# Kernel optimization log

Hardware: AMD Instinct MI355X
Metric: run time of the kernel (lower is better)

The kernel has to match this reference:

```python
import jax, jax.numpy as jnp
import numpy as np

DEPTH = 6
B, D, E, H = 8192, 256, 256, 50
N_INNER = (1 << (DEPTH - 1)) - 1   # 31
N_LEAF = 1 << (DEPTH - 1)          # 32


def setup_inputs() -> dict:
    key = jax.random.key(0)
    ks = jax.random.split(key, 16)
    g = lambda k, shape, fan: (jax.random.normal(k, shape, dtype=jnp.float32)
                               / jnp.sqrt(jnp.float32(fan)))
    return {
        "x": jax.random.normal(ks[0], (B, D), dtype=jnp.float32),
        "enc_W": g(ks[1], (4, E, E), E),
        "enc_b": jnp.zeros((4, E), jnp.float32),
        # inner nodes, stacked over N_INNER
        "in_W1": g(ks[2], (N_INNER, E, H), E),
        "in_b1": jnp.zeros((N_INNER, H), jnp.float32),
        "in_Ww": g(ks[3], (N_INNER, H, D), H),
        "in_bw": jnp.zeros((N_INNER, D), jnp.float32),
        "in_Wb": g(ks[4], (N_INNER, H), H),
        "in_bb": jnp.zeros((N_INNER,), jnp.float32),
        "in_Wbeta": g(ks[5], (N_INNER, H), H),
        "in_bbeta": jnp.zeros((N_INNER,), jnp.float32),
        # leaf models, stacked over N_LEAF
        "lf_W1": g(ks[6], (N_LEAF, E, E), E),
        "lf_b1": jnp.zeros((N_LEAF, E), jnp.float32),
        "lf_W2": g(ks[7], (N_LEAF, E), E),
        "lf_b2": jnp.zeros((N_LEAF,), jnp.float32),
    }


def reference(x, enc_W, enc_b, in_W1, in_b1, in_Ww, in_bw, in_Wb, in_bb,
              in_Wbeta, in_bbeta, lf_W1, lf_b1, lf_W2, lf_b2):
    batch = x.shape[0]
    # encoder: 4 relu Dense layers
    emb = x
    for i in range(4):
        emb = jax.nn.relu(emb @ enc_W[i] + enc_b[i])

    # all inner-node gates in one batched pass  -> pR: [N_INNER, B]
    h = jax.nn.relu(jnp.einsum('be,neh->nbh', emb, in_W1) + in_b1[:, None, :])
    w = jax.nn.softmax(jnp.einsum('nbh,nhd->nbd', h, in_Ww) + in_bw[:, None, :], axis=-1)
    b = jnp.einsum('nbh,nh->nb', h, in_Wb) + in_bb[:, None]
    beta = jnp.einsum('nbh,nh->nb', h, in_Wbeta) + in_bbeta[:, None]
    pR = jax.nn.sigmoid(beta * (jnp.einsum('nbd,bd->nb', w, x) + b))

    # all leaf MLPs in one batched pass  -> y_leaf: [N_LEAF, B]
    hl = jax.nn.relu(jnp.einsum('be,leh->lbh', emb, lf_W1) + lf_b1[:, None, :])
    y_leaf = jnp.einsum('lbh,lh->lb', hl, lf_W2) + lf_b2[:, None]

    # path probabilities (heap ordering; right child weighted by pR)
    prob = jnp.ones((batch, 1), dtype=x.dtype)
    idx = 0
    for level in range(DEPTH - 1):
        cnt = 1 << level
        p = pR[idx:idx + cnt].T                       # [B, cnt]
        prob = jnp.stack([prob * (1.0 - p), prob * p], axis=-1).reshape(batch, 2 * cnt)
        idx += cnt

    return jnp.sum(prob * y_leaf.T, axis=1, keepdims=True)  # [B, 1]
```

## Files before the change

kernel.cpp:

```cpp
#include <hip/hip_runtime.h>


#define B_ROWS 8192
#define HDIM 50
#define HPAD 64

typedef _Float16 f16;
typedef _Float16 f16x8 __attribute__((ext_vector_type(8)));
typedef _Float16 f16x4 __attribute__((ext_vector_type(4)));
typedef float f32x4 __attribute__((ext_vector_type(4)));

static __device__ __forceinline__ f32x4 mfma16(f16x8 a, f16x8 b, f32x4 c) {
  return __builtin_amdgcn_mfma_f32_16x16x32_f16(a, b, c, 0, 0, 0);
}

static __device__ __forceinline__ void gload16(const void* g, void* l) {
  __builtin_amdgcn_global_load_lds(
      (const __attribute__((address_space(1))) unsigned int*)g,
      (__attribute__((address_space(3))) unsigned int*)l, 16, 0, 0);
}

__global__ void k_cast_f16(const float* __restrict__ in, f16* __restrict__ out, int n4) {
  int i = blockIdx.x * blockDim.x + threadIdx.x;
  if (i < n4) {
    float4 v = reinterpret_cast<const float4*>(in)[i];
    f16x4 o = { (f16)v.x, (f16)v.y, (f16)v.z, (f16)v.w };
    reinterpret_cast<f16x4*>(out)[i] = o;
  }
}

__global__ void k_tcast(const float* __restrict__ in, f16* __restrict__ out,
                        int R, int C, int Rp, int Cp) {
  __shared__ float t[32][33];
  const int s = blockIdx.z;
  const int r0 = blockIdx.x * 32, c0 = blockIdx.y * 32;
  const int tx = threadIdx.x, ty = threadIdx.y;
  const float* ip = in + (size_t)s * R * C;
  f16* op = out + (size_t)s * Cp * Rp;
#pragma unroll
  for (int i = 0; i < 4; ++i) {
    int r = r0 + ty + 8 * i, c = c0 + tx;
    t[ty + 8 * i][tx] = (r < R && c < C) ? ip[(size_t)r * C + c] : 0.f;
  }
  __syncthreads();
#pragma unroll
  for (int i = 0; i < 4; ++i) {
    int c = c0 + ty + 8 * i, r = r0 + tx;
    if (c < Cp && r < Rp) op[(size_t)c * Rp + r] = (f16)t[tx][ty + 8 * i];
  }
}

__global__ __launch_bounds__(256) void k_enc4(const float* __restrict__ x,
    const f16* __restrict__ encWT, const float* __restrict__ enc_b,
    f16* __restrict__ emb) {
  __shared__ f16 act[2][32][264];
  __shared__ f16 Bt[256][72];
  const int tid = threadIdx.x;
  const int wave = tid >> 6, lane = tid & 63;
  const int grp = lane >> 4, lid = lane & 15;
  const int row0 = blockIdx.x * 32;
  const int sr = tid >> 3, sc = (tid & 7) * 8;

  {
    const int xr = tid >> 3, xc = (tid & 7) * 32;
    const float* src = x + (size_t)(row0 + xr) * 256 + xc;
#pragma unroll
    for (int j = 0; j < 4; ++j) {
      float4 a = ((const float4*)src)[2 * j];
      float4 b = ((const float4*)src)[2 * j + 1];
      f16x8 o = { (f16)a.x, (f16)a.y, (f16)a.z, (f16)a.w,
                  (f16)b.x, (f16)b.y, (f16)b.z, (f16)b.w };
      *(f16x8*)&act[0][xr][xc + 8 * j] = o;
    }
  }
  __syncthreads();

  for (int l = 0; l < 4; ++l) {
    const int cur = l & 1, nxt = cur ^ 1;
    f32x4 acc[2][4] = {};
    for (int kt = 0; kt < 4; ++kt) {
#pragma unroll
      for (int p = 0; p < 8; ++p)
        *(f16x8*)&Bt[p * 32 + sr][sc] =
            *(const f16x8*)&encWT[(size_t)l * 65536 + (size_t)(p * 32 + sr) * 256 + kt * 64 + sc];
      __syncthreads();
#pragma unroll
      for (int kk = 0; kk < 2; ++kk) {
        f16x8 af[2], bf[4];
#pragma unroll
        for (int m = 0; m < 2; ++m)
          af[m] = *(const f16x8*)&act[cur][m * 16 + lid][kt * 64 + kk * 32 + grp * 8];
#pragma unroll
        for (int n = 0; n < 4; ++n)
          bf[n] = *(const f16x8*)&Bt[wave * 64 + n * 16 + lid][kk * 32 + grp * 8];
#pragma unroll
        for (int m = 0; m < 2; ++m)
#pragma unroll
          for (int n = 0; n < 4; ++n) acc[m][n] = mfma16(af[m], bf[n], acc[m][n]);
      }
      __syncthreads();
    }
#pragma unroll
    for (int n = 0; n < 4; ++n) {
      const int col = wave * 64 + n * 16 + lid;
      const float bv = enc_b[l * 256 + col];
#pragma unroll
      for (int m = 0; m < 2; ++m)
#pragma unroll
        for (int r = 0; r < 4; ++r) {
          float v = acc[m][n][r] + bv;
          act[nxt][m * 16 + grp * 4 + r][col] = (f16)(v > 0.f ? v : 0.f);
        }
    }
    __syncthreads();
  }
  {
    const int xr = tid >> 3, xc = (tid & 7) * 32;
#pragma unroll
    for (int j = 0; j < 4; ++j)
      *(f16x8*)&emb[(size_t)(row0 + xr) * 256 + xc + 8 * j] =
          *(const f16x8*)&act[0][xr][xc + 8 * j];
  }
}

__global__ __launch_bounds__(256, 2) void k_inner(const f16* __restrict__ emb,
    const f16* __restrict__ W1T_all, const float* __restrict__ b1_all,
    const f16* __restrict__ WwT_all, const f16* __restrict__ x_h,
    const float* __restrict__ bw_all, const float* __restrict__ Wb_all,
    const float* __restrict__ bb_all, const float* __restrict__ Wbeta_all,
    const float* __restrict__ bbeta_all, float* __restrict__ pR) {
  __shared__ f16 et[64][264];
  __shared__ f16 hbuf[4][64][72];
  __shared__ float bbuf[4][64], betabuf[4][64];

  const int tid = threadIdx.x;
  const int wave = tid >> 6, lane = tid & 63;
  const int grp = lane >> 4, lid = lane & 15;
  const int row0 = blockIdx.x * 64;
  const int node = blockIdx.y * 4 + wave;

  {
    const int r = tid >> 2, cb = (tid & 3) * 64;
#pragma unroll
    for (int j = 0; j < 8; ++j)
      *(f16x8*)&et[r][cb + 8 * j] =
          *(const f16x8*)&emb[(size_t)(row0 + r) * 256 + cb + 8 * j];
  }
  __syncthreads();
  if (node >= 31) return;

  const f16* W1T = W1T_all + (size_t)node * HPAD * 256;
  const f16* WwT = WwT_all + (size_t)node * 256 * HPAD;

  f32x4 acc1[4][4] = {};
  f16x8 wf[2][4];
#pragma unroll
  for (int h4 = 0; h4 < 4; ++h4)
    wf[0][h4] = *(const f16x8*)&W1T[(size_t)(h4 * 16 + lid) * 256 + grp * 8];
  for (int kt = 0; kt < 8; ++kt) {
    const int cur = kt & 1, nxt = cur ^ 1;
    if (kt < 7) {
#pragma unroll
      for (int h4 = 0; h4 < 4; ++h4)
        wf[nxt][h4] = *(const f16x8*)&W1T[(size_t)(h4 * 16 + lid) * 256 +
                                          (kt + 1) * 32 + grp * 8];
    }
    f16x8 af[4];
#pragma unroll
    for (int m = 0; m < 4; ++m)
      af[m] = *(const f16x8*)&et[m * 16 + lid][kt * 32 + grp * 8];
#pragma unroll
    for (int h4 = 0; h4 < 4; ++h4)
#pragma unroll
      for (int m = 0; m < 4; ++m)
        acc1[h4][m] = mfma16(wf[cur][h4], af[m], acc1[h4][m]);
  }
#pragma unroll
  for (int h4 = 0; h4 < 4; ++h4) {
    const int hc = h4 * 16 + grp * 4;
    float bva[4];
#pragma unroll
    for (int r = 0; r < 4; ++r)
      bva[r] = (hc + r < HDIM) ? b1_all[node * HDIM + hc + r] : 0.f;
#pragma unroll
    for (int m = 0; m < 4; ++m) {
      f16x4 hv;
#pragma unroll
      for (int r = 0; r < 4; ++r) {
        float v = acc1[h4][m][r] + bva[r];
        hv[r] = (f16)(v > 0.f ? v : 0.f);
      }
      *(f16x4*)&hbuf[wave][m * 16 + lid][hc] = hv;
    }
  }

  {
    float sb = 0.f, sbt = 0.f;
#pragma unroll
    for (int v8 = 0; v8 < 7; ++v8) {
      f16x8 hv = *(const f16x8*)&hbuf[wave][lane][v8 * 8];
#pragma unroll
      for (int j = 0; j < 8; ++j) {
        const int c = v8 * 8 + j;
        if (c < HDIM) {
          float hvf = (float)hv[j];
          sb  += hvf * Wb_all[node * HDIM + c];
          sbt += hvf * Wbeta_all[node * HDIM + c];
        }
      }
    }
    bbuf[wave][lane] = sb + bb_all[node];
    betabuf[wave][lane] = sbt + bbeta_all[node];
  }

  float s[4] = {0.f, 0.f, 0.f, 0.f}, dt[4] = {0.f, 0.f, 0.f, 0.f};
  for (int c = 0; c < 4; ++c) {
    f16x8 awf[2][4];
#pragma unroll
    for (int kk = 0; kk < 2; ++kk)
#pragma unroll
      for (int n4 = 0; n4 < 4; ++n4)
        awf[kk][n4] = *(const f16x8*)&WwT[(size_t)(c * 64 + n4 * 16 + lid) * HPAD +
                                          kk * 32 + grp * 8];
    f32x4 acc2[4][4] = {};
#pragma unroll
    for (int kk = 0; kk < 2; ++kk) {
      f16x8 hf[4];
#pragma unroll
      for (int m = 0; m < 4; ++m)
        hf[m] = *(const f16x8*)&hbuf[wave][m * 16 + lid][kk * 32 + grp * 8];
#pragma unroll
      for (int n4 = 0; n4 < 4; ++n4)
#pragma unroll
        for (int m = 0; m < 4; ++m)
          acc2[n4][m] = mfma16(awf[kk][n4], hf[m], acc2[n4][m]);
    }
#pragma unroll
    for (int n4 = 0; n4 < 4; ++n4) {
      float4 bwv = *(const float4*)&bw_all[node * 256 + c * 64 + n4 * 16 + grp * 4];
      float bwa[4] = {bwv.x, bwv.y, bwv.z, bwv.w};
#pragma unroll
      for (int m = 0; m < 4; ++m) {
        f16x4 xv = *(const f16x4*)&x_h[(size_t)(row0 + m * 16 + lid) * 256 +
                                       c * 64 + n4 * 16 + grp * 4];
#pragma unroll
        for (int r = 0; r < 4; ++r) {
          float e = __expf(acc2[n4][m][r] + bwa[r]);
          s[m] += e;
          dt[m] += e * (float)xv[r];
        }
      }
    }
  }
#pragma unroll
  for (int m = 0; m < 4; ++m) {
    s[m]  += __shfl_xor(s[m], 16, 64);  s[m]  += __shfl_xor(s[m], 32, 64);
    dt[m] += __shfl_xor(dt[m], 16, 64); dt[m] += __shfl_xor(dt[m], 32, 64);
  }
  if (grp == 0) {
#pragma unroll
    for (int m = 0; m < 4; ++m) {
      const int row = m * 16 + lid;
      float z = betabuf[wave][row] * (dt[m] / s[m] + bbuf[wave][row]);
      pR[(size_t)(row0 + row) * 32 + node] = 1.f / (1.f + __expf(-z));
    }
  }
}

__global__ __launch_bounds__(512) void k_leaf(const f16* __restrict__ emb,
    const f16* __restrict__ W1T_all, const float* __restrict__ b1_all,
    const float* __restrict__ W2_all, const float* __restrict__ b2_all,
    float* __restrict__ y_leaf) {
  __shared__ f16 Alds[128 * 64];
  __shared__ f16 Blds[256 * 64];
  __shared__ float red[4][128];
  const int tid = threadIdx.x;
  const int wave = tid >> 6, lane = tid & 63;
  const int wm = wave >> 2, wn = wave & 3;
  const int grp = lane >> 4, lid = lane & 15;
  const int row0 = blockIdx.x * 128;
  const int leaf = blockIdx.y;
  const f16* WT = W1T_all + (size_t)leaf * 65536;
  const float* b1 = b1_all + leaf * 256;
  const float* W2 = W2_all + leaf * 256;

  const int lrow = lane >> 3;
  const int sslot = (lane & 7) ^ lrow;

  f32x4 acc[4][4] = {};
  const int swzA = (lid & 7);
  for (int kt = 0; kt < 4; ++kt) {
#pragma unroll
    for (int r2 = 0; r2 < 2; ++r2) {
      const int arow = r2 * 64 + wave * 8 + lrow;
      gload16(emb + (size_t)(row0 + arow) * 256 + kt * 64 + sslot * 8,
              (char*)Alds + r2 * 8192 + wave * 1024);
    }
#pragma unroll
    for (int r4 = 0; r4 < 4; ++r4) {
      const int brow = r4 * 64 + wave * 8 + lrow;
      gload16(WT + (size_t)brow * 256 + kt * 64 + sslot * 8,
              (char*)Blds + r4 * 8192 + wave * 1024);
    }
    __syncthreads();
#pragma unroll
    for (int kk = 0; kk < 2; ++kk) {
      f16x8 af[4], bf[4];
#pragma unroll
      for (int rb = 0; rb < 4; ++rb) {
        const int row = wm * 64 + rb * 16 + lid;
        af[rb] = *(const f16x8*)((const char*)Alds + row * 128 +
                                 (((kk * 4 + grp) ^ swzA) << 4));
      }
#pragma unroll
      for (int cb = 0; cb < 4; ++cb) {
        const int row = wn * 64 + cb * 16 + lid;
        bf[cb] = *(const f16x8*)((const char*)Blds + row * 128 +
                                 (((kk * 4 + grp) ^ swzA) << 4));
      }
#pragma unroll
      for (int cb = 0; cb < 4; ++cb)
#pragma unroll
        for (int rb = 0; rb < 4; ++rb)
          acc[cb][rb] = mfma16(bf[cb], af[rb], acc[cb][rb]);
    }
    __syncthreads();
  }
  float b1a[4][4], w2a[4][4];
#pragma unroll
  for (int cb = 0; cb < 4; ++cb) {
    float4 t1 = *(const float4*)&b1[wn * 64 + cb * 16 + grp * 4];
    float4 t2 = *(const float4*)&W2[wn * 64 + cb * 16 + grp * 4];
    b1a[cb][0] = t1.x; b1a[cb][1] = t1.y; b1a[cb][2] = t1.z; b1a[cb][3] = t1.w;
    w2a[cb][0] = t2.x; w2a[cb][1] = t2.y; w2a[cb][2] = t2.z; w2a[cb][3] = t2.w;
  }
  float rs[4] = {0.f, 0.f, 0.f, 0.f};
#pragma unroll
  for (int cb = 0; cb < 4; ++cb)
#pragma unroll
    for (int rb = 0; rb < 4; ++rb)
#pragma unroll
      for (int r = 0; r < 4; ++r) {
        float v = acc[cb][rb][r] + b1a[cb][r];
        v = v > 0.f ? v : 0.f;
        rs[rb] += v * w2a[cb][r];
      }
#pragma unroll
  for (int rb = 0; rb < 4; ++rb) {
    rs[rb] += __shfl_xor(rs[rb], 16, 64);
    rs[rb] += __shfl_xor(rs[rb], 32, 64);
  }
  if (lane < 16)
#pragma unroll
    for (int rb = 0; rb < 4; ++rb)
      red[wn][wm * 64 + rb * 16 + lane] = rs[rb];
  __syncthreads();
  if (tid < 128) {
    float y = red[0][tid] + red[1][tid] + red[2][tid] + red[3][tid] + b2_all[leaf];
    y_leaf[(size_t)(row0 + tid) * 32 + leaf] = y;
  }
}

__global__ void k_combine(const float* __restrict__ pR, const float* __restrict__ y_leaf,
                          float* __restrict__ out) {
  const int b = blockIdx.x * 256 + threadIdx.x;
  float p[32], y[32];
  const float4* pp = (const float4*)(pR + (size_t)b * 32);
  const float4* yp = (const float4*)(y_leaf + (size_t)b * 32);
#pragma unroll
  for (int i = 0; i < 8; ++i) {
    float4 v = pp[i]; p[i*4] = v.x; p[i*4+1] = v.y; p[i*4+2] = v.z; p[i*4+3] = v.w;
    float4 w = yp[i]; y[i*4] = w.x; y[i*4+1] = w.y; y[i*4+2] = w.z; y[i*4+3] = w.w;
  }
  float o = 0.f;
#pragma unroll
  for (int l = 0; l < 32; ++l) {
    float pr = 1.f;
    int node = 0;
#pragma unroll
    for (int k = 0; k < 5; ++k) {
      const int bit = (l >> (4 - k)) & 1;
      const float pv = p[node];
      pr *= bit ? pv : (1.f - pv);
      node = 2 * node + 1 + bit;
    }
    o += pr * y[l];
  }
  out[b] = o;
}

extern "C" void kernel_launch(void* const* d_in, const int* in_sizes, int n_in,
                              void* d_out, int out_size, void* d_ws, size_t ws_size,
                              hipStream_t stream) {
  (void)in_sizes; (void)n_in; (void)out_size; (void)ws_size;
  const float* x        = (const float*)d_in[0];
  const float* enc_W    = (const float*)d_in[1];
  const float* enc_b    = (const float*)d_in[2];
  const float* in_W1    = (const float*)d_in[3];
  const float* in_b1    = (const float*)d_in[4];
  const float* in_Ww    = (const float*)d_in[5];
  const float* in_bw    = (const float*)d_in[6];
  const float* in_Wb    = (const float*)d_in[7];
  const float* in_bb    = (const float*)d_in[8];
  const float* in_Wbeta = (const float*)d_in[9];
  const float* in_bbeta = (const float*)d_in[10];
  const float* lf_W1    = (const float*)d_in[11];
  const float* lf_b1    = (const float*)d_in[12];
  const float* lf_W2    = (const float*)d_in[13];
  const float* lf_b2    = (const float*)d_in[14];
  float* out = (float*)d_out;

  char* ws = (char*)d_ws;
  f16* x_h     = (f16*)(ws);
  f16* emb     = (f16*)(ws + 4194304);
  f16* encWT   = (f16*)(ws + 8388608);
  f16* lfW1T   = (f16*)(ws + 8912896);
  f16* inW1T   = (f16*)(ws + 13107200);
  f16* inWwT   = (f16*)(ws + 14123008);
  float* pR    = (float*)(ws + 15138816);
  float* y_leaf= (float*)(ws + 16187392);

  dim3 tb(32, 8);
  hipLaunchKernelGGL(k_cast_f16, dim3(2048), dim3(256), 0, stream, x, x_h, B_ROWS * 256 / 4);
  hipLaunchKernelGGL(k_tcast, dim3(8, 8, 4),  tb, 0, stream, enc_W, encWT, 256, 256, 256, 256);
  hipLaunchKernelGGL(k_tcast, dim3(8, 8, 32), tb, 0, stream, lf_W1, lfW1T, 256, 256, 256, 256);
  hipLaunchKernelGGL(k_tcast, dim3(8, 2, 31), tb, 0, stream, in_W1, inW1T, 256, 50, 256, 64);
  hipLaunchKernelGGL(k_tcast, dim3(2, 8, 31), tb, 0, stream, in_Ww, inWwT, 50, 256, 64, 256);

  hipLaunchKernelGGL(k_enc4, dim3(256), dim3(256), 0, stream, x, encWT, enc_b, emb);
  hipLaunchKernelGGL(k_inner, dim3(128, 8), dim3(256), 0, stream, emb, inW1T, in_b1,
                     inWwT, x_h, in_bw, in_Wb, in_bb, in_Wbeta, in_bbeta, pR);
  hipLaunchKernelGGL(k_leaf, dim3(64, 32), dim3(512), 0, stream, emb, lfW1T, lf_b1, lf_W2, lf_b2, y_leaf);
  hipLaunchKernelGGL(k_combine, dim3(32), dim3(256), 0, stream, pR, y_leaf, out);
}
```

Baseline: 232.3 us.

## Fold gate heads into MFMA, stage x in LDS, double-buffer larger leaf tiles

The inner-node kernel now computes the b and beta heads as an extra MFMA tile, using a prepacked weight block that appends the Wb and Wbeta rows to the transposed Ww. This replaces the scalar per-lane dot product. It also stages the x tile into the emb LDS buffer so the softmax dot product reads LDS instead of global memory, and keeps the padded waves alive until the final barrier. The leaf kernel doubles its row tile to 256 and double-buffers the async global-to-LDS loads so the next k-slice loads while the current one computes. The cost is more LDS use (about 130KB in the leaf kernel) and more accumulator registers, which may lower occupancy.

```diff
diff --git a/kernel.cpp b/kernel.cpp
--- a/kernel.cpp
+++ b/kernel.cpp
@@ -47,6 +47,32 @@
   for (int i = 0; i < 4; ++i) {
     int c = c0 + ty + 8 * i, r = r0 + tx;
     if (c < Cp && r < Rp) op[(size_t)c * Rp + r] = (f16)t[tx][ty + 8 * i];
+  }
+}
+
+__global__ void k_prep_ww(const float* __restrict__ Ww, const float* __restrict__ Wb,
+                          const float* __restrict__ Wbeta, f16* __restrict__ WwE) {
+  const int node = blockIdx.x;
+  const int d = threadIdx.x;
+  f16 row[64];
+#pragma unroll
+  for (int h = 0; h < 64; ++h)
+    row[h] = (h < HDIM) ? (f16)Ww[((size_t)node * HDIM + h) * 256 + d] : (f16)0.f;
+  f16* dst = WwE + (size_t)node * 272 * 64 + (size_t)d * 64;
+#pragma unroll
+  for (int j = 0; j < 8; ++j) *(f16x8*)&dst[j * 8] = *(const f16x8*)&row[j * 8];
+  if (d < 16) {
+    f16 er[64];
+#pragma unroll
+    for (int h = 0; h < 64; ++h) {
+      float v = 0.f;
+      if (d == 0 && h < HDIM) v = Wb[node * HDIM + h];
+      if (d == 1 && h < HDIM) v = Wbeta[node * HDIM + h];
+      er[h] = (f16)v;
+    }
+    f16* dst2 = WwE + (size_t)node * 272 * 64 + (size_t)(256 + d) * 64;
+#pragma unroll
+    for (int j = 0; j < 8; ++j) *(f16x8*)&dst2[j * 8] = *(const f16x8*)&er[j * 8];
   }
 }
 
@@ -125,19 +151,18 @@
 
 __global__ __launch_bounds__(256, 2) void k_inner(const f16* __restrict__ emb,
     const f16* __restrict__ W1T_all, const float* __restrict__ b1_all,
-    const f16* __restrict__ WwT_all, const f16* __restrict__ x_h,
-    const float* __restrict__ bw_all, const float* __restrict__ Wb_all,
-    const float* __restrict__ bb_all, const float* __restrict__ Wbeta_all,
+    const f16* __restrict__ WwE_all, const f16* __restrict__ x_h,
+    const float* __restrict__ bw_all, const float* __restrict__ bb_all,
     const float* __restrict__ bbeta_all, float* __restrict__ pR) {
   __shared__ f16 et[64][264];
   __shared__ f16 hbuf[4][64][72];
-  __shared__ float bbuf[4][64], betabuf[4][64];
 
   const int tid = threadIdx.x;
   const int wave = tid >> 6, lane = tid & 63;
   const int grp = lane >> 4, lid = lane & 15;
   const int row0 = blockIdx.x * 64;
-  const int node = blockIdx.y * 4 + wave;
+  const int node_raw = blockIdx.y * 4 + wave;
+  const int node = node_raw < 31 ? node_raw : 30;
 
   {
     const int r = tid >> 2, cb = (tid & 3) * 64;
@@ -147,10 +172,9 @@
           *(const f16x8*)&emb[(size_t)(row0 + r) * 256 + cb + 8 * j];
   }
   __syncthreads();
-  if (node >= 31) return;
 
   const f16* W1T = W1T_all + (size_t)node * HPAD * 256;
-  const f16* WwT = WwT_all + (size_t)node * 256 * HPAD;
+  const f16* WwE = WwE_all + (size_t)node * 272 * 64;
 
   f32x4 acc1[4][4] = {};
   f16x8 wf[2][4];
@@ -193,24 +217,25 @@
       *(f16x4*)&hbuf[wave][m * 16 + lid][hc] = hv;
     }
   }
-
+  __syncthreads();
   {
-    float sb = 0.f, sbt = 0.f;
-#pragma unroll
-    for (int v8 = 0; v8 < 7; ++v8) {
-      f16x8 hv = *(const f16x8*)&hbuf[wave][lane][v8 * 8];
-#pragma unroll
-      for (int j = 0; j < 8; ++j) {
-        const int c = v8 * 8 + j;
-        if (c < HDIM) {
-          float hvf = (float)hv[j];
-          sb  += hvf * Wb_all[node * HDIM + c];
-          sbt += hvf * Wbeta_all[node * HDIM + c];
-        }
-      }
-    }
-    bbuf[wave][lane] = sb + bb_all[node];
-    betabuf[wave][lane] = sbt + bbeta_all[node];
+    const int r = tid >> 2, cb = (tid & 3) * 64;
+#pragma unroll
+    for (int j = 0; j < 8; ++j)
+      *(f16x8*)&et[r][cb + 8 * j] =
+          *(const f16x8*)&x_h[(size_t)(row0 + r) * 256 + cb + 8 * j];
+  }
+  __syncthreads();
+
+  f32x4 accm[4] = {};
+#pragma unroll
+  for (int kk = 0; kk < 2; ++kk) {
+    f16x8 wmini = *(const f16x8*)&WwE[(size_t)(256 + lid) * 64 + kk * 32 + grp * 8];
+#pragma unroll
+    for (int m = 0; m < 4; ++m) {
+      f16x8 hf = *(const f16x8*)&hbuf[wave][m * 16 + lid][kk * 32 + grp * 8];
+      accm[m] = mfma16(wmini, hf, accm[m]);
+    }
   }
 
   float s[4] = {0.f, 0.f, 0.f, 0.f}, dt[4] = {0.f, 0.f, 0.f, 0.f};
@@ -220,7 +245,7 @@
     for (int kk = 0; kk < 2; ++kk)
 #pragma unroll
       for (int n4 = 0; n4 < 4; ++n4)
-        awf[kk][n4] = *(const f16x8*)&WwT[(size_t)(c * 64 + n4 * 16 + lid) * HPAD +
+        awf[kk][n4] = *(const f16x8*)&WwE[(size_t)(c * 64 + n4 * 16 + lid) * 64 +
                                           kk * 32 + grp * 8];
     f32x4 acc2[4][4] = {};
 #pragma unroll
@@ -241,8 +266,7 @@
       float bwa[4] = {bwv.x, bwv.y, bwv.z, bwv.w};
 #pragma unroll
       for (int m = 0; m < 4; ++m) {
-        f16x4 xv = *(const f16x4*)&x_h[(size_t)(row0 + m * 16 + lid) * 256 +
-                                       c * 64 + n4 * 16 + grp * 4];
+        f16x4 xv = *(const f16x4*)&et[m * 16 + lid][c * 64 + n4 * 16 + grp * 4];
 #pragma unroll
         for (int r = 0; r < 4; ++r) {
           float e = __expf(acc2[n4][m][r] + bwa[r]);
@@ -257,11 +281,14 @@
     s[m]  += __shfl_xor(s[m], 16, 64);  s[m]  += __shfl_xor(s[m], 32, 64);
     dt[m] += __shfl_xor(dt[m], 16, 64); dt[m] += __shfl_xor(dt[m], 32, 64);
   }
-  if (grp == 0) {
+  if (grp == 0 && node_raw < 31) {
+    const float bbv = bb_all[node], bbetav = bbeta_all[node];
 #pragma unroll
     for (int m = 0; m < 4; ++m) {
       const int row = m * 16 + lid;
-      float z = betabuf[wave][row] * (dt[m] / s[m] + bbuf[wave][row]);
+      float b = accm[m][0] + bbv;
+      float beta = accm[m][1] + bbetav;
+      float z = beta * (dt[m] / s[m] + b);
       pR[(size_t)(row0 + row) * 32 + node] = 1.f / (1.f + __expf(-z));
     }
   }
@@ -271,14 +298,14 @@
     const f16* __restrict__ W1T_all, const float* __restrict__ b1_all,
     const float* __restrict__ W2_all, const float* __restrict__ b2_all,
     float* __restrict__ y_leaf) {
-  __shared__ f16 Alds[128 * 64];
-  __shared__ f16 Blds[256 * 64];
-  __shared__ float red[4][128];
+  __shared__ f16 Albuf[2][256 * 64];
+  __shared__ f16 Blbuf[2][256 * 64];
+  __shared__ float red[4][256];
   const int tid = threadIdx.x;
   const int wave = tid >> 6, lane = tid & 63;
   const int wm = wave >> 2, wn = wave & 3;
   const int grp = lane >> 4, lid = lane & 15;
-  const int row0 = blockIdx.x * 128;
+  const int row0 = blockIdx.x * 256;
   const int leaf = blockIdx.y;
   const f16* WT = W1T_all + (size_t)leaf * 65536;
   const float* b1 = b1_all + leaf * 256;
@@ -286,45 +313,48 @@
 
   const int lrow = lane >> 3;
   const int sslot = (lane & 7) ^ lrow;
-
-  f32x4 acc[4][4] = {};
   const int swzA = (lid & 7);
+
+#define LEAF_STAGE(buf, kt)                                                    \
+  {                                                                            \
+    _Pragma("unroll")                                                          \
+    for (int r4 = 0; r4 < 4; ++r4) {                                           \
+      const int rr = r4 * 64 + wave * 8 + lrow;                                \
+      gload16(emb + (size_t)(row0 + rr) * 256 + (kt) * 64 + sslot * 8,         \
+              (char*)&Albuf[buf][0] + r4 * 8192 + wave * 1024);                \
+      gload16(WT + (size_t)rr * 256 + (kt) * 64 + sslot * 8,                   \
+              (char*)&Blbuf[buf][0] + r4 * 8192 + wave * 1024);                \
+    }                                                                          \
+  }
+
+  f32x4 acc[4][8] = {};
+  LEAF_STAGE(0, 0);
+  __syncthreads();
   for (int kt = 0; kt < 4; ++kt) {
-#pragma unroll
-    for (int r2 = 0; r2 < 2; ++r2) {
-      const int arow = r2 * 64 + wave * 8 + lrow;
-      gload16(emb + (size_t)(row0 + arow) * 256 + kt * 64 + sslot * 8,
-              (char*)Alds + r2 * 8192 + wave * 1024);
-    }
-#pragma unroll
-    for (int r4 = 0; r4 < 4; ++r4) {
-      const int brow = r4 * 64 + wave * 8 + lrow;
-      gload16(WT + (size_t)brow * 256 + kt * 64 + sslot * 8,
-              (char*)Blds + r4 * 8192 + wave * 1024);
-    }
-    __syncthreads();
+    const int b = kt & 1;
+    if (kt < 3) LEAF_STAGE(b ^ 1, kt + 1);
 #pragma unroll
     for (int kk = 0; kk < 2; ++kk) {
-      f16x8 af[4], bf[4];
-#pragma unroll
-      for (int rb = 0; rb < 4; ++rb) {
-        const int row = wm * 64 + rb * 16 + lid;
-        af[rb] = *(const f16x8*)((const char*)Alds + row * 128 +
+      f16x8 af[8], bf[4];
+#pragma unroll
+      for (int rb = 0; rb < 8; ++rb) {
+        const int row = wm * 128 + rb * 16 + lid;
+        af[rb] = *(const f16x8*)((const char*)&Albuf[b][0] + row * 128 +
                                  (((kk * 4 + grp) ^ swzA) << 4));
       }
 #pragma unroll
       for (int cb = 0; cb < 4; ++cb) {
-        const int row = wn * 64 + cb * 16 + lid;
-        bf[cb] = *(const f16x8*)((const char*)Blds + row * 128 +
+        const int col = wn * 64 + cb * 16 + lid;
+        bf[cb] = *(const f16x8*)((const char*)&Blbuf[b][0] + col * 128 +
                                  (((kk * 4 + grp) ^ swzA) << 4));
       }
 #pragma unroll
       for (int cb = 0; cb < 4; ++cb)
 #pragma unroll
-        for (int rb = 0; rb < 4; ++rb)
+        for (int rb = 0; rb < 8; ++rb)
           acc[cb][rb] = mfma16(bf[cb], af[rb], acc[cb][rb]);
     }
-    __syncthreads();
+    if (kt < 3) __syncthreads();
   }
   float b1a[4][4], w2a[4][4];
 #pragma unroll
@@ -334,11 +364,11 @@
     b1a[cb][0] = t1.x; b1a[cb][1] = t1.y; b1a[cb][2] = t1.z; b1a[cb][3] = t1.w;
     w2a[cb][0] = t2.x; w2a[cb][1] = t2.y; w2a[cb][2] = t2.z; w2a[cb][3] = t2.w;
   }
-  float rs[4] = {0.f, 0.f, 0.f, 0.f};
+  float rs[8] = {};
 #pragma unroll
   for (int cb = 0; cb < 4; ++cb)
 #pragma unroll
-    for (int rb = 0; rb < 4; ++rb)
+    for (int rb = 0; rb < 8; ++rb)
 #pragma unroll
       for (int r = 0; r < 4; ++r) {
         float v = acc[cb][rb][r] + b1a[cb][r];
@@ -346,16 +376,17 @@
         rs[rb] += v * w2a[cb][r];
       }
 #pragma unroll
-  for (int rb = 0; rb < 4; ++rb) {
+  for (int rb = 0; rb < 8; ++rb) {
     rs[rb] += __shfl_xor(rs[rb], 16, 64);
     rs[rb] += __shfl_xor(rs[rb], 32, 64);
   }
+  __syncthreads();
   if (lane < 16)
 #pragma unroll
-    for (int rb = 0; rb < 4; ++rb)
-      red[wn][wm * 64 + rb * 16 + lane] = rs[rb];
-  __syncthreads();
-  if (tid < 128) {
+    for (int rb = 0; rb < 8; ++rb)
+      red[wn][wm * 128 + rb * 16 + lane] = rs[rb];
+  __syncthreads();
+  if (tid < 256) {
     float y = red[0][tid] + red[1][tid] + red[2][tid] + red[3][tid] + b2_all[leaf];
     y_leaf[(size_t)(row0 + tid) * 32 + leaf] = y;
   }
@@ -416,20 +447,20 @@
   f16* encWT   = (f16*)(ws + 8388608);
   f16* lfW1T   = (f16*)(ws + 8912896);
   f16* inW1T   = (f16*)(ws + 13107200);
-  f16* inWwT   = (f16*)(ws + 14123008);
-  float* pR    = (float*)(ws + 15138816);
-  float* y_leaf= (float*)(ws + 16187392);
+  f16* WwE     = (f16*)(ws + 14123008);
+  float* pR    = (float*)(ws + 15202304);
+  float* y_leaf= (float*)(ws + 16250880);
 
   dim3 tb(32, 8);
   hipLaunchKernelGGL(k_cast_f16, dim3(2048), dim3(256), 0, stream, x, x_h, B_ROWS * 256 / 4);
   hipLaunchKernelGGL(k_tcast, dim3(8, 8, 4),  tb, 0, stream, enc_W, encWT, 256, 256, 256, 256);
   hipLaunchKernelGGL(k_tcast, dim3(8, 8, 32), tb, 0, stream, lf_W1, lfW1T, 256, 256, 256, 256);
   hipLaunchKernelGGL(k_tcast, dim3(8, 2, 31), tb, 0, stream, in_W1, inW1T, 256, 50, 256, 64);
-  hipLaunchKernelGGL(k_tcast, dim3(2, 8, 31), tb, 0, stream, in_Ww, inWwT, 50, 256, 64, 256);
+  hipLaunchKernelGGL(k_prep_ww, dim3(31), dim3(256), 0, stream, in_Ww, in_Wb, in_Wbeta, WwE);
 
   hipLaunchKernelGGL(k_enc4, dim3(256), dim3(256), 0, stream, x, encWT, enc_b, emb);
   hipLaunchKernelGGL(k_inner, dim3(128, 8), dim3(256), 0, stream, emb, inW1T, in_b1,
-                     inWwT, x_h, in_bw, in_Wb, in_bb, in_Wbeta, in_bbeta, pR);
-  hipLaunchKernelGGL(k_leaf, dim3(64, 32), dim3(512), 0, stream, emb, lfW1T, lf_b1, lf_W2, lf_b2, y_leaf);
+                     WwE, x_h, in_bw, in_bb, in_bbeta, pR);
+  hipLaunchKernelGGL(k_leaf, dim3(32, 32), dim3(512), 0, stream, emb, lfW1T, lf_b1, lf_W2, lf_b2, y_leaf);
   hipLaunchKernelGGL(k_combine, dim3(32), dim3(256), 0, stream, pR, y_leaf, out);
 }
```

Result: faster. 214.9 us (-7.5%).
